# Optimization experiments

Hardware: AMD Instinct MI355X
Metric: run time of the kernel (lower is better)

## Reference

```python
import jax, jax.numpy as jnp
import numpy as np

B, S, D, H, DK = 2, 2048, 2048, 16, 128
ALIBI_SLOPE = 8.0
NEG = -1e9  # finite stand-in for -inf so gradients stay finite


def setup_inputs() -> dict:
    key = jax.random.key(0)
    ks = jax.random.split(key, 8)
    states = jax.random.normal(ks[0], (B, S, D), jnp.float32)
    # causal ALiBi-style additive bias: -(i-j) for j<=i else very negative
    pos = jnp.arange(S)
    dist = pos[None, :] - pos[:, None]  # j - i
    bias = jnp.where(dist <= 0, dist.astype(jnp.float32), NEG)
    bias_mask = jnp.broadcast_to(bias[None], (B, S, S))
    # per-head scale: exp2(-((h+1)*slope/H))
    head_scale = jnp.exp2(-((jnp.arange(H) + 1.0) * ALIBI_SLOPE / H)).astype(jnp.float32)
    init = lambda k, shp: jax.random.normal(k, shp, jnp.float32) * (shp[-1] ** -0.5)
    return {
        'states': states,
        'bias_mask': bias_mask,
        'head_scale': head_scale,
        'Wq': init(ks[1], (D, D)), 'bq': jnp.zeros((D,), jnp.float32),
        'Wk': init(ks[2], (D, D)), 'bk': jnp.zeros((D,), jnp.float32),
        'Wv': init(ks[3], (D, D)), 'bv': jnp.zeros((D,), jnp.float32),
        'Wg': init(ks[4], (H, D)), 'bg': jnp.zeros((H,), jnp.float32),
        'Wo': init(ks[5], (D, D)), 'bo': jnp.zeros((D,), jnp.float32),
    }


def reference(states, bias_mask, head_scale, Wq, bq, Wk, bk, Wv, bv, Wg, bg, Wo, bo):
    b, s, d = states.shape
    key_scale = DK ** -0.5
    proj = lambda x, W, bias: x @ W.T + bias
    # [b,s,d] -> [b,h,s,dk]
    q = proj(states, Wq, bq).reshape(b, s, H, DK).transpose(0, 2, 1, 3)
    k = proj(states, Wk, bk).reshape(b, s, H, DK).transpose(0, 2, 1, 3)
    v = proj(states, Wv, bv).reshape(b, s, H, DK).transpose(0, 2, 1, 3)
    # additive per-head ALiBi bias: [b,1,s,s] * [1,h,1,1]
    bias = bias_mask[:, None, :, :] * head_scale[None, :, None, None]
    scores = jnp.einsum('bhqd,bhkd->bhqk', q, k) * key_scale + bias
    attn = jax.nn.softmax(scores, axis=-1)
    o = jnp.einsum('bhqk,bhkd->bhqd', attn, v).transpose(0, 2, 1, 3)  # [b,s,h,dk]
    g = jax.nn.sigmoid(proj(states, Wg, bg))  # [b,s,h]
    o = o * g[..., None]
    return proj(o.reshape(b, s, d), Wo, bo)
```

## Files before the change

kernel.cpp:

```cpp
#include <hip/hip_runtime.h>

#define SEQ  2048
#define NROW 4096
#define KDIM 2048
#define NH   16
#define DKH  128
#define CSUB 20.0f
#define LOG2E 1.44269504088896f

typedef unsigned int u32;
typedef unsigned short u16;
typedef __attribute__((ext_vector_type(8))) __bf16 bf16x8;
typedef __attribute__((ext_vector_type(4))) float f32x4;
typedef __attribute__((ext_vector_type(4))) u16 u16x4;

struct alignas(16) U4 { u32 x, y, z, w; };

__device__ __forceinline__ u16 f2bf(float f) {
  u32 u = __builtin_bit_cast(u32, f);
  u32 r = (u + 0x7fffu + ((u >> 16) & 1u)) >> 16;
  return (u16)r;
}
__device__ __forceinline__ u16 f2bf_n(float f) {
  __bf16 h = (__bf16)f;
  return __builtin_bit_cast(u16, h);
}
__device__ __forceinline__ bf16x8 asb(U4 v) { return __builtin_bit_cast(bf16x8, v); }
__device__ __forceinline__ float exp2a(float x) {
  float r;
  asm("v_exp_f32 %0, %1" : "=v"(r) : "v"(x));
  return r;
}

__device__ __forceinline__ void gl2lds16(const u16* g, u16* l) {
  __builtin_amdgcn_global_load_lds(
      (const __attribute__((address_space(1))) void*)g,
      (__attribute__((address_space(3))) void*)l, 16, 0, 0);
}

__global__ __launch_bounds__(256)
void cvtk(const float* __restrict__ src, u16* __restrict__ dst, int n)
{
  const int i = (blockIdx.x * 256 + threadIdx.x) * 4;
  if (i < n) {
    f32x4 v = *(const f32x4*)(src + i);
    u16x4 o;
#pragma unroll
    for (int j = 0; j < 4; ++j) o[j] = f2bf_n(v[j]);
    *(u16x4*)(dst + i) = o;
  }
}

__global__ __launch_bounds__(256)
void cvt3k(const float* __restrict__ s0, const float* __restrict__ s1,
           const float* __restrict__ s2, u16* __restrict__ dst, int n)
{
  const float* s = blockIdx.y == 0 ? s0 : (blockIdx.y == 1 ? s1 : s2);
  u16* d = dst + (size_t)blockIdx.y * n;
  const int i = (blockIdx.x * 256 + threadIdx.x) * 4;
  if (i < n) {
    f32x4 v = *(const f32x4*)(s + i);
    u16x4 o;
#pragma unroll
    for (int j = 0; j < 4; ++j) o[j] = f2bf_n(v[j]);
    *(u16x4*)(d + i) = o;
  }
}

__global__ __launch_bounds__(512, 2)
void qkvg(const u16* __restrict__ A, const u16* __restrict__ B,
          const float* __restrict__ bq, const float* __restrict__ bk,
          const float* __restrict__ bv, u16* __restrict__ Qw,
          u16* __restrict__ Kw, u16* __restrict__ Vw)
{
  __shared__ alignas(16) u16 As[2][256 * 64];
  __shared__ alignas(16) u16 Bs[2][256 * 64];
  const int tid = threadIdx.x;
  const int lane = tid & 63, wave = tid >> 6;
  const int wm = wave >> 2, wn = wave & 3;
  const int l15 = lane & 15, quad = lane >> 4;
  const int l7 = l15 & 7;
  const int m0 = blockIdx.y * 256, n0 = blockIdx.x * 256;

  const int srow = wave * 8 + (lane >> 3);
  const int scol = ((lane & 7) ^ (lane >> 3)) * 8;

  f32x4 acc[8][4];
#pragma unroll
  for (int i = 0; i < 8; ++i)
#pragma unroll
    for (int j = 0; j < 4; ++j) acc[i][j] = {0.f, 0.f, 0.f, 0.f};

#define QSTAGE(kt, buf)                                                      \
  do {                                                                       \
    const int koff_ = (kt) * 64;                                             \
    _Pragma("unroll")                                                        \
    for (int j = 0; j < 4; ++j) {                                            \
      gl2lds16(A + (size_t)(m0 + j * 64 + srow) * KDIM + koff_ + scol,       \
               &As[buf][(j * 64 + wave * 8) * 64]);                          \
      gl2lds16(B + (size_t)(n0 + j * 64 + srow) * KDIM + koff_ + scol,       \
               &Bs[buf][(j * 64 + wave * 8) * 64]);                          \
    }                                                                        \
  } while (0)

  QSTAGE(0, 0);
  QSTAGE(1, 1);

  const int NT = KDIM / 64;
  for (int kt = 0; kt < NT; ++kt) {
    const int cb = kt & 1;
    if (kt + 1 < NT) asm volatile("s_waitcnt vmcnt(8)" ::: "memory");
    else             asm volatile("s_waitcnt vmcnt(0)" ::: "memory");
    asm volatile("s_barrier" ::: "memory");

    U4 bf[4][2];
#pragma unroll
    for (int nf = 0; nf < 4; ++nf)
#pragma unroll
      for (int kf = 0; kf < 2; ++kf)
        bf[nf][kf] = *(const U4*)(&Bs[cb][(wn * 64 + nf * 16 + l15) * 64 +
                                          (((kf * 4 + quad) ^ l7) * 8)]);
    __builtin_amdgcn_s_setprio(1);
#pragma unroll
    for (int p = 0; p < 4; ++p) {
      U4 af[2][2];
#pragma unroll
      for (int mi = 0; mi < 2; ++mi)
#pragma unroll
        for (int kf = 0; kf < 2; ++kf)
          af[mi][kf] = *(const U4*)(&As[cb][(wm * 128 + (p * 2 + mi) * 16 + l15) * 64 +
                                            (((kf * 4 + quad) ^ l7) * 8)]);
#pragma unroll
      for (int mi = 0; mi < 2; ++mi)
#pragma unroll
        for (int nf = 0; nf < 4; ++nf)
#pragma unroll
          for (int kf = 0; kf < 2; ++kf)
            acc[p * 2 + mi][nf] = __builtin_amdgcn_mfma_f32_16x16x32_bf16(
                asb(af[mi][kf]), asb(bf[nf][kf]), acc[p * 2 + mi][nf], 0, 0, 0);
    }
    __builtin_amdgcn_s_setprio(0);
    asm volatile("s_barrier" ::: "memory");
    if (kt + 2 < NT) QSTAGE(kt + 2, cb);
  }
#undef QSTAGE

  const int seg = n0 >> 11;
  const float* bp = seg == 0 ? bq : (seg == 1 ? bk : bv);
  u16* Cq = seg == 0 ? Qw : Kw;

#pragma unroll
  for (int mf = 0; mf < 8; ++mf) {
    const int rowb = m0 + wm * 128 + mf * 16 + quad * 4;
    const int b = rowb >> 11, sr = rowb & (SEQ - 1);
#pragma unroll
    for (int nf = 0; nf < 4; ++nf) {
      const int col6 = n0 + wn * 64 + nf * 16 + l15;
      const int col = col6 & 2047;
      const int h = col >> 7, dk = col & 127;
      const float bvl = bp[col];
      if (seg == 2) {
        u16x4 pk;
#pragma unroll
        for (int r = 0; r < 4; ++r) pk[r] = f2bf_n(acc[mf][nf][r] + bvl);
        *(u16x4*)(Vw + ((size_t)(b * NH + h) * DKH + dk) * SEQ + sr) = pk;
      } else {
#pragma unroll
        for (int r = 0; r < 4; ++r)
          Cq[((size_t)(b * NH + h) * SEQ + (sr + r)) * DKH + dk] =
              f2bf_n(acc[mf][nf][r] + bvl);
      }
    }
  }
}

__device__ __forceinline__ void stage_ab(const u16* __restrict__ A,
                                         const u16* __restrict__ B,
                                         int m0, int n0, int kk,
                                         u16* Asb, u16* Bsb,
                                         int wave, int gr, int gc)
{
#pragma unroll
  for (int it = 0; it < 2; ++it) {
    const int r0 = wave * 32 + it * 16;
    gl2lds16(A + (size_t)(m0 + r0 + gr) * KDIM + kk + gc, Asb + r0 * 32);
    gl2lds16(B + (size_t)(n0 + r0 + gr) * KDIM + kk + gc, Bsb + r0 * 32);
  }
}

__global__ __launch_bounds__(256, 2)
void gemm_bt(const u16* __restrict__ A, const u16* __restrict__ B,
             const float* __restrict__ bias, float* __restrict__ Cf)
{
  __shared__ alignas(16) u16 As[128 * 32];
  __shared__ alignas(16) u16 Bs[128 * 32];
  const int tid = threadIdx.x;
  const int lane = tid & 63, wave = tid >> 6;
  const int wm = wave >> 1, wn = wave & 1;
  const int l15 = lane & 15, quad = lane >> 4;
  const int m0 = blockIdx.y * 128, n0 = blockIdx.x * 128;

  f32x4 acc[4][4];
#pragma unroll
  for (int i = 0; i < 4; ++i)
#pragma unroll
    for (int j = 0; j < 4; ++j) acc[i][j] = {0.f, 0.f, 0.f, 0.f};

  const int gr = lane >> 2;
  const int gc = (lane & 3) * 8;

  for (int kk = 0; kk < KDIM; kk += 32) {
    stage_ab(A, B, m0, n0, kk, As, Bs, wave, gr, gc);
    __syncthreads();
    U4 af[4], bg[4];
#pragma unroll
    for (int t = 0; t < 4; ++t) {
      af[t] = *(const U4*)(As + (wm * 64 + t * 16 + l15) * 32 + quad * 8);
      bg[t] = *(const U4*)(Bs + (wn * 64 + t * 16 + l15) * 32 + quad * 8);
    }
#pragma unroll
    for (int mt = 0; mt < 4; ++mt)
#pragma unroll
      for (int nt = 0; nt < 4; ++nt)
        acc[mt][nt] = __builtin_amdgcn_mfma_f32_16x16x32_bf16(
            asb(af[mt]), asb(bg[nt]), acc[mt][nt], 0, 0, 0);
    __syncthreads();
  }

#pragma unroll
  for (int mt = 0; mt < 4; ++mt) {
    const int rowb = m0 + wm * 64 + mt * 16 + quad * 4;
#pragma unroll
    for (int nt = 0; nt < 4; ++nt) {
      const int col = n0 + wn * 64 + nt * 16 + l15;
      const float bv = bias[col];
#pragma unroll
      for (int r = 0; r < 4; ++r)
        Cf[(size_t)(rowb + r) * KDIM + col] = acc[mt][nt][r] + bv;
    }
  }
}

__global__ __launch_bounds__(256)
void gateg(const u16* __restrict__ X, const float* __restrict__ Wg,
           const float* __restrict__ bg, float* __restrict__ G)
{
  __shared__ float red[4][16][16];
  const int tid = threadIdx.x;
  const int lane = tid & 63, wave = tid >> 6;
  const int l15 = lane & 15, quad = lane >> 4;
  const int m0 = blockIdx.x * 16;

  const u16*  Xp = X + (size_t)(m0 + l15) * KDIM + wave * 512 + quad * 8;
  const float* Wp = Wg + (size_t)l15 * KDIM + wave * 512 + quad * 8;

  f32x4 acc = {0.f, 0.f, 0.f, 0.f};
#pragma unroll
  for (int kk = 0; kk < 512; kk += 32) {
    U4 a = *(const U4*)(Xp + kk);
    f32x4 w0 = *(const f32x4*)(Wp + kk);
    f32x4 w1 = *(const f32x4*)(Wp + kk + 4);
    U4 bw;
    bw.x = (u32)f2bf_n(w0[0]) | ((u32)f2bf_n(w0[1]) << 16);
    bw.y = (u32)f2bf_n(w0[2]) | ((u32)f2bf_n(w0[3]) << 16);
    bw.z = (u32)f2bf_n(w1[0]) | ((u32)f2bf_n(w1[1]) << 16);
    bw.w = (u32)f2bf_n(w1[2]) | ((u32)f2bf_n(w1[3]) << 16);
    acc = __builtin_amdgcn_mfma_f32_16x16x32_bf16(asb(a), asb(bw), acc, 0, 0, 0);
  }
#pragma unroll
  for (int r = 0; r < 4; ++r) red[wave][quad * 4 + r][l15] = acc[r];
  __syncthreads();
  const int row = tid >> 4, head = tid & 15;
  float s = bg[head];
#pragma unroll
  for (int w = 0; w < 4; ++w) s += red[w][row][head];
  G[(size_t)(m0 + row) * NH + head] = 1.f / (1.f + __expf(-s));
}

__device__ __forceinline__ void stage_kv(const u16* __restrict__ Kh,
                                         const u16* __restrict__ Vh,
                                         int kk, u16* Ksb, u16* Vsb,
                                         int wave, int lane)
{
  const int rK = lane >> 4, cK = lane & 15;
  const int rV = lane >> 3, cV = lane & 7;
#pragma unroll
  for (int j = 0; j < 4; ++j) {
    const int r0k = wave * 16 + j * 4;
    const int xk = ((j & 1) << 2) | rK;
    gl2lds16(Kh + (size_t)(kk + r0k + rK) * DKH + ((cK ^ xk) * 8),
             Ksb + r0k * 128);
    const int r0v = wave * 32 + j * 8;
    gl2lds16(Vh + (size_t)(r0v + rV) * SEQ + kk + ((cV ^ rV) * 8),
             Vsb + r0v * 64);
  }
}

__global__ __launch_bounds__(256, 2)
void attnk(const u16* __restrict__ Q, const u16* __restrict__ Km,
           const u16* __restrict__ Vt, const float* __restrict__ hsc,
           const float* __restrict__ G, u16* __restrict__ O)
{
  __shared__ alignas(16) u16 Ks[2][64 * 128];
  __shared__ alignas(16) u16 Vs[2][128 * 64];
  __shared__ alignas(16) u16 Ps[4][16 * 72];
  const int tid = threadIdx.x;
  const int lane = tid & 63, wave = tid >> 6;
  const int l15 = lane & 15, quad = lane >> 4;
  const int l7x = l15 & 7;
  const int qt = 31 - blockIdx.y, bh = blockIdx.x;
  const int b = bh >> 4, h = bh & 15;
  const size_t hoff = (size_t)bh * SEQ * DKH;
  const u16* Qh = Q + hoff;
  const u16* Kh = Km + hoff;
  const u16* Vh = Vt + hoff;
  const float hs2 = hsc[h] * LOG2E;
  const float ks2 = 0.08838834764831845f * LOG2E;
  const float csub2 = CSUB * LOG2E;
  const float dstep = 64.0f * hs2;

  const int q0 = qt * 64 + wave * 16;
  const int ntile = qt + 1;

  U4 aq[4];
#pragma unroll
  for (int c = 0; c < 4; ++c)
    aq[c] = *(const U4*)(Qh + (size_t)(q0 + l15) * DKH + c * 32 + quad * 8);

  float base[4][4];
#pragma unroll
  for (int r = 0; r < 4; ++r) {
    const int i = q0 + quad * 4 + r;
#pragma unroll
    for (int nt = 0; nt < 4; ++nt)
      base[r][nt] = (float)(nt * 16 + l15 - i) * hs2 - csub2;
  }

  f32x4 oacc[8];
#pragma unroll
  for (int c = 0; c < 8; ++c) oacc[c] = {0.f, 0.f, 0.f, 0.f};
  float l_lane[4] = {0.f, 0.f, 0.f, 0.f};

  stage_kv(Kh, Vh, 0, Ks[0], Vs[0], wave, lane);

  for (int t = 0; t < ntile; ++t) {
    const int kk = t * 64;
    const int cb = t & 1;
    __syncthreads();
    if (t + 1 < ntile)
      stage_kv(Kh, Vh, kk + 64, Ks[cb ^ 1], Vs[cb ^ 1], wave, lane);

    f32x4 sf[4];
#pragma unroll
    for (int nt = 0; nt < 4; ++nt) {
      f32x4 s = {0.f, 0.f, 0.f, 0.f};
#pragma unroll
      for (int c = 0; c < 4; ++c) {
        U4 bk = *(const U4*)(Ks[cb] + (nt * 16 + l15) * 128 +
                             (((c * 4 + quad) ^ l7x) * 8));
        s = __builtin_amdgcn_mfma_f32_16x16x32_bf16(asb(aq[c]), asb(bk), s, 0, 0, 0);
      }
      sf[nt] = s;
    }

    u16* Pw = &Ps[wave][0];
    const float tf = (float)t;
    if (t + 1 < ntile) {
#pragma unroll
      for (int r = 0; r < 4; ++r) {
#pragma unroll
        for (int nt = 0; nt < 4; ++nt) {
          const float p = exp2a(fmaf(sf[nt][r], ks2, fmaf(tf, dstep, base[r][nt])));
          l_lane[r] += p;
          Pw[(quad * 4 + r) * 72 + nt * 16 + l15] = f2bf_n(p);
        }
      }
    } else {
#pragma unroll
      for (int r = 0; r < 4; ++r) {
        const int i = q0 + quad * 4 + r;
#pragma unroll
        for (int nt = 0; nt < 4; ++nt) {
          const int j = kk + nt * 16 + l15;
          float p = 0.f;
          if (j <= i)
            p = exp2a(fmaf(sf[nt][r], ks2, fmaf(tf, dstep, base[r][nt])));
          l_lane[r] += p;
          Pw[(quad * 4 + r) * 72 + nt * 16 + l15] = f2bf_n(p);
        }
      }
    }
    asm volatile("s_waitcnt lgkmcnt(0)" ::: "memory");
    __builtin_amdgcn_sched_barrier(0);
    U4 pf0 = *(const U4*)(Pw + l15 * 72 + quad * 8);
    U4 pf1 = *(const U4*)(Pw + l15 * 72 + 32 + quad * 8);
#pragma unroll
    for (int c = 0; c < 8; ++c) {
      U4 bv0 = *(const U4*)(Vs[cb] + (c * 16 + l15) * 64 + ((quad ^ l7x) * 8));
      U4 bv1 = *(const U4*)(Vs[cb] + (c * 16 + l15) * 64 + (((quad + 4) ^ l7x) * 8));
      oacc[c] = __builtin_amdgcn_mfma_f32_16x16x32_bf16(asb(pf0), asb(bv0), oacc[c], 0, 0, 0);
      oacc[c] = __builtin_amdgcn_mfma_f32_16x16x32_bf16(asb(pf1), asb(bv1), oacc[c], 0, 0, 0);
    }
  }

  float sc[4];
#pragma unroll
  for (int r = 0; r < 4; ++r) {
#pragma unroll
    for (int d = 1; d < 16; d <<= 1)
      l_lane[r] += __shfl_xor(l_lane[r], d, 64);
    const int i = q0 + quad * 4 + r;
    sc[r] = G[(size_t)(b * SEQ + i) * NH + h] / l_lane[r];
  }

  __syncthreads();
  u16* OL = &Ks[0][0] + wave * 2112;
#pragma unroll
  for (int c = 0; c < 8; ++c)
#pragma unroll
    for (int r = 0; r < 4; ++r)
      OL[(quad * 4 + r) * 132 + c * 16 + l15] = f2bf_n(oacc[c][r] * sc[r]);
  __syncthreads();
#pragma unroll
  for (int o = 0; o < 4; ++o) {
    const int row = o * 4 + quad;
    U4 val = *(const U4*)(OL + row * 132 + l15 * 8);
    *(U4*)(O + ((size_t)(b * SEQ + q0 + row) * NH + h) * DKH + l15 * 8) = val;
  }
}

extern "C" void kernel_launch(void* const* d_in, const int* in_sizes, int n_in,
                              void* d_out, int out_size, void* d_ws, size_t ws_size,
                              hipStream_t stream)
{
  const float* states = (const float*)d_in[0];
  const float* hscale = (const float*)d_in[2];
  const float* Wq = (const float*)d_in[3];
  const float* bq = (const float*)d_in[4];
  const float* Wk = (const float*)d_in[5];
  const float* bk = (const float*)d_in[6];
  const float* Wv = (const float*)d_in[7];
  const float* bv = (const float*)d_in[8];
  const float* Wg = (const float*)d_in[9];
  const float* bg = (const float*)d_in[10];
  const float* Wo = (const float*)d_in[11];
  const float* bo = (const float*)d_in[12];
  float* out = (float*)d_out;

  char* ws = (char*)d_ws;
  const size_t MB = 1024 * 1024;
  u16* S16  = (u16*)(ws);
  u16* Qw   = (u16*)(ws + 16 * MB);
  u16* Kw   = (u16*)(ws + 32 * MB);
  u16* Vw   = (u16*)(ws + 48 * MB);
  u16* W16  = (u16*)(ws + 64 * MB);
  u16* Ow   = (u16*)(ws + 64 * MB);
  u16* Wo16 = (u16*)(ws + 80 * MB);
  float* Gw = out;

  const int NW = KDIM * KDIM;
  const int NS = NROW * KDIM;
  dim3 blk(256);

  cvtk<<<dim3(NS / 1024), blk, 0, stream>>>(states, S16, NS);
  gateg<<<dim3(NROW / 16), blk, 0, stream>>>(S16, Wg, bg, Gw);
  cvt3k<<<dim3(NW / 1024, 3), blk, 0, stream>>>(Wq, Wk, Wv, W16, NW);
  qkvg<<<dim3(24, 16), dim3(512), 0, stream>>>(S16, W16, bq, bk, bv, Qw, Kw, Vw);
  attnk<<<dim3(32, 32), blk, 0, stream>>>(Qw, Kw, Vw, hscale, Gw, Ow);
  cvtk<<<dim3(NW / 1024), blk, 0, stream>>>(Wo, Wo16, NW);
  gemm_bt<<<dim3(16, 32), blk, 0, stream>>>(Ow, Wo16, bo, out);
}
```

Baseline: 426.2 us.

## Unify QKV and output GEMMs into triple-buffered 256x128 kernel

Replaces the 256x256 double-buffered QKV GEMM and the simple 128x128 single-buffered output GEMM with one 8-wave 256x128 kernel. It uses a three-stage LDS ring and interleaves the next-tile global-to-LDS loads with the MFMA loop. A mode flag selects either the head-scattered bf16 QKV epilogue or the fp32 bias epilogue. The output projection gains prefetching and swizzled LDS, while the QKV GEMM gets smaller tiles, more blocks and a smaller register footprint, at the cost of more A-tile refetching.

```diff
diff --git a/kernel.cpp b/kernel.cpp
--- a/kernel.cpp
+++ b/kernel.cpp
@@ -68,137 +68,30 @@
 }
 
 __global__ __launch_bounds__(512, 2)
-void qkvg(const u16* __restrict__ A, const u16* __restrict__ B,
-          const float* __restrict__ bq, const float* __restrict__ bk,
-          const float* __restrict__ bv, u16* __restrict__ Qw,
-          u16* __restrict__ Kw, u16* __restrict__ Vw)
-{
-  __shared__ alignas(16) u16 As[2][256 * 64];
-  __shared__ alignas(16) u16 Bs[2][256 * 64];
-  const int tid = threadIdx.x;
-  const int lane = tid & 63, wave = tid >> 6;
-  const int wm = wave >> 2, wn = wave & 3;
-  const int l15 = lane & 15, quad = lane >> 4;
-  const int l7 = l15 & 7;
-  const int m0 = blockIdx.y * 256, n0 = blockIdx.x * 256;
-
-  const int srow = wave * 8 + (lane >> 3);
-  const int scol = ((lane & 7) ^ (lane >> 3)) * 8;
-
-  f32x4 acc[8][4];
-#pragma unroll
-  for (int i = 0; i < 8; ++i)
-#pragma unroll
-    for (int j = 0; j < 4; ++j) acc[i][j] = {0.f, 0.f, 0.f, 0.f};
-
-#define QSTAGE(kt, buf)                                                      \
-  do {                                                                       \
-    const int koff_ = (kt) * 64;                                             \
-    _Pragma("unroll")                                                        \
-    for (int j = 0; j < 4; ++j) {                                            \
-      gl2lds16(A + (size_t)(m0 + j * 64 + srow) * KDIM + koff_ + scol,       \
-               &As[buf][(j * 64 + wave * 8) * 64]);                          \
-      gl2lds16(B + (size_t)(n0 + j * 64 + srow) * KDIM + koff_ + scol,       \
-               &Bs[buf][(j * 64 + wave * 8) * 64]);                          \
-    }                                                                        \
-  } while (0)
-
-  QSTAGE(0, 0);
-  QSTAGE(1, 1);
-
-  const int NT = KDIM / 64;
-  for (int kt = 0; kt < NT; ++kt) {
-    const int cb = kt & 1;
-    if (kt + 1 < NT) asm volatile("s_waitcnt vmcnt(8)" ::: "memory");
-    else             asm volatile("s_waitcnt vmcnt(0)" ::: "memory");
-    asm volatile("s_barrier" ::: "memory");
-
-    U4 bf[4][2];
-#pragma unroll
-    for (int nf = 0; nf < 4; ++nf)
-#pragma unroll
-      for (int kf = 0; kf < 2; ++kf)
-        bf[nf][kf] = *(const U4*)(&Bs[cb][(wn * 64 + nf * 16 + l15) * 64 +
-                                          (((kf * 4 + quad) ^ l7) * 8)]);
-    __builtin_amdgcn_s_setprio(1);
-#pragma unroll
-    for (int p = 0; p < 4; ++p) {
-      U4 af[2][2];
-#pragma unroll
-      for (int mi = 0; mi < 2; ++mi)
-#pragma unroll
-        for (int kf = 0; kf < 2; ++kf)
-          af[mi][kf] = *(const U4*)(&As[cb][(wm * 128 + (p * 2 + mi) * 16 + l15) * 64 +
-                                            (((kf * 4 + quad) ^ l7) * 8)]);
-#pragma unroll
-      for (int mi = 0; mi < 2; ++mi)
-#pragma unroll
-        for (int nf = 0; nf < 4; ++nf)
-#pragma unroll
-          for (int kf = 0; kf < 2; ++kf)
-            acc[p * 2 + mi][nf] = __builtin_amdgcn_mfma_f32_16x16x32_bf16(
-                asb(af[mi][kf]), asb(bf[nf][kf]), acc[p * 2 + mi][nf], 0, 0, 0);
-    }
-    __builtin_amdgcn_s_setprio(0);
-    asm volatile("s_barrier" ::: "memory");
-    if (kt + 2 < NT) QSTAGE(kt + 2, cb);
-  }
-#undef QSTAGE
-
-  const int seg = n0 >> 11;
-  const float* bp = seg == 0 ? bq : (seg == 1 ? bk : bv);
-  u16* Cq = seg == 0 ? Qw : Kw;
-
-#pragma unroll
-  for (int mf = 0; mf < 8; ++mf) {
-    const int rowb = m0 + wm * 128 + mf * 16 + quad * 4;
-    const int b = rowb >> 11, sr = rowb & (SEQ - 1);
-#pragma unroll
-    for (int nf = 0; nf < 4; ++nf) {
-      const int col6 = n0 + wn * 64 + nf * 16 + l15;
-      const int col = col6 & 2047;
-      const int h = col >> 7, dk = col & 127;
-      const float bvl = bp[col];
-      if (seg == 2) {
-        u16x4 pk;
-#pragma unroll
-        for (int r = 0; r < 4; ++r) pk[r] = f2bf_n(acc[mf][nf][r] + bvl);
-        *(u16x4*)(Vw + ((size_t)(b * NH + h) * DKH + dk) * SEQ + sr) = pk;
-      } else {
-#pragma unroll
-        for (int r = 0; r < 4; ++r)
-          Cq[((size_t)(b * NH + h) * SEQ + (sr + r)) * DKH + dk] =
-              f2bf_n(acc[mf][nf][r] + bvl);
-      }
-    }
-  }
-}
-
-__device__ __forceinline__ void stage_ab(const u16* __restrict__ A,
-                                         const u16* __restrict__ B,
-                                         int m0, int n0, int kk,
-                                         u16* Asb, u16* Bsb,
-                                         int wave, int gr, int gc)
-{
-#pragma unroll
-  for (int it = 0; it < 2; ++it) {
-    const int r0 = wave * 32 + it * 16;
-    gl2lds16(A + (size_t)(m0 + r0 + gr) * KDIM + kk + gc, Asb + r0 * 32);
-    gl2lds16(B + (size_t)(n0 + r0 + gr) * KDIM + kk + gc, Bsb + r0 * 32);
-  }
-}
-
-__global__ __launch_bounds__(256, 2)
-void gemm_bt(const u16* __restrict__ A, const u16* __restrict__ B,
-             const float* __restrict__ bias, float* __restrict__ Cf)
-{
-  __shared__ alignas(16) u16 As[128 * 32];
-  __shared__ alignas(16) u16 Bs[128 * 32];
+void gemm8p(const u16* __restrict__ A, const u16* __restrict__ B,
+            const float* __restrict__ bq, const float* __restrict__ bk,
+            const float* __restrict__ bv, u16* __restrict__ Qw,
+            u16* __restrict__ Kw, u16* __restrict__ Vw,
+            float* __restrict__ Cf, int mode)
+{
+  __shared__ alignas(16) u16 As[3][256 * 64];
+  __shared__ alignas(16) u16 Bs[3][128 * 64];
   const int tid = threadIdx.x;
   const int lane = tid & 63, wave = tid >> 6;
   const int wm = wave >> 1, wn = wave & 1;
   const int l15 = lane & 15, quad = lane >> 4;
-  const int m0 = blockIdx.y * 128, n0 = blockIdx.x * 128;
+  const int l7 = l15 & 7;
+  const int m0 = blockIdx.y * 256, n0 = blockIdx.x * 128;
+
+  const int sr8 = lane >> 3;
+  const int scol = ((lane & 7) ^ sr8) * 8;
+
+#define STG_A(kt, buf, j)                                                    \
+  gl2lds16(A + (size_t)(m0 + (j) * 64 + wave * 8 + sr8) * KDIM + (kt) * 64 + scol, \
+           &As[buf][((j) * 64 + wave * 8) * 64])
+#define STG_B(kt, buf, j)                                                    \
+  gl2lds16(B + (size_t)(n0 + (j) * 64 + wave * 8 + sr8) * KDIM + (kt) * 64 + scol, \
+           &Bs[buf][((j) * 64 + wave * 8) * 64])
 
   f32x4 acc[4][4];
 #pragma unroll
@@ -206,37 +99,93 @@
 #pragma unroll
     for (int j = 0; j < 4; ++j) acc[i][j] = {0.f, 0.f, 0.f, 0.f};
 
-  const int gr = lane >> 2;
-  const int gc = (lane & 3) * 8;
-
-  for (int kk = 0; kk < KDIM; kk += 32) {
-    stage_ab(A, B, m0, n0, kk, As, Bs, wave, gr, gc);
-    __syncthreads();
-    U4 af[4], bg[4];
-#pragma unroll
-    for (int t = 0; t < 4; ++t) {
-      af[t] = *(const U4*)(As + (wm * 64 + t * 16 + l15) * 32 + quad * 8);
-      bg[t] = *(const U4*)(Bs + (wn * 64 + t * 16 + l15) * 32 + quad * 8);
-    }
-#pragma unroll
-    for (int mt = 0; mt < 4; ++mt)
-#pragma unroll
-      for (int nt = 0; nt < 4; ++nt)
-        acc[mt][nt] = __builtin_amdgcn_mfma_f32_16x16x32_bf16(
-            asb(af[mt]), asb(bg[nt]), acc[mt][nt], 0, 0, 0);
-    __syncthreads();
-  }
-
-#pragma unroll
-  for (int mt = 0; mt < 4; ++mt) {
-    const int rowb = m0 + wm * 64 + mt * 16 + quad * 4;
-#pragma unroll
-    for (int nt = 0; nt < 4; ++nt) {
-      const int col = n0 + wn * 64 + nt * 16 + l15;
-      const float bv = bias[col];
-#pragma unroll
-      for (int r = 0; r < 4; ++r)
-        Cf[(size_t)(rowb + r) * KDIM + col] = acc[mt][nt][r] + bv;
+  STG_A(0, 0, 0); STG_A(0, 0, 1); STG_A(0, 0, 2); STG_A(0, 0, 3);
+  STG_B(0, 0, 0); STG_B(0, 0, 1);
+  STG_A(1, 1, 0); STG_A(1, 1, 1); STG_A(1, 1, 2); STG_A(1, 1, 3);
+  STG_B(1, 1, 0); STG_B(1, 1, 1);
+
+  const int NT = KDIM / 64;
+  for (int kt = 0; kt < NT; ++kt) {
+    const int cb = kt % 3;
+    const int sb = (kt + 2) % 3;
+    if (kt + 1 < NT) asm volatile("s_waitcnt vmcnt(6)" ::: "memory");
+    else             asm volatile("s_waitcnt vmcnt(0)" ::: "memory");
+    asm volatile("s_barrier" ::: "memory");
+    __builtin_amdgcn_sched_barrier(0);
+    const bool st = (kt + 2) < NT;
+
+    U4 bf[4][2];
+#pragma unroll
+    for (int nf = 0; nf < 4; ++nf)
+#pragma unroll
+      for (int kf = 0; kf < 2; ++kf)
+        bf[nf][kf] = *(const U4*)(&Bs[cb][(wn * 64 + nf * 16 + l15) * 64 +
+                                          (((kf * 4 + quad) ^ l7) * 8)]);
+
+#pragma unroll
+    for (int mf = 0; mf < 4; ++mf) {
+      if (st) {
+        if (mf == 0) { STG_A(kt + 2, sb, 0); STG_A(kt + 2, sb, 1); }
+        else if (mf == 1) { STG_A(kt + 2, sb, 2); STG_A(kt + 2, sb, 3); }
+        else if (mf == 2) { STG_B(kt + 2, sb, 0); STG_B(kt + 2, sb, 1); }
+      }
+      U4 af[2];
+#pragma unroll
+      for (int kf = 0; kf < 2; ++kf)
+        af[kf] = *(const U4*)(&As[cb][(wm * 64 + mf * 16 + l15) * 64 +
+                                      (((kf * 4 + quad) ^ l7) * 8)]);
+      __builtin_amdgcn_s_setprio(1);
+#pragma unroll
+      for (int nf = 0; nf < 4; ++nf)
+#pragma unroll
+        for (int kf = 0; kf < 2; ++kf)
+          acc[mf][nf] = __builtin_amdgcn_mfma_f32_16x16x32_bf16(
+              asb(af[kf]), asb(bf[nf][kf]), acc[mf][nf], 0, 0, 0);
+      __builtin_amdgcn_s_setprio(0);
+    }
+  }
+#undef STG_A
+#undef STG_B
+
+  if (mode == 0) {
+#pragma unroll
+    for (int mf = 0; mf < 4; ++mf) {
+      const int rowb = m0 + wm * 64 + mf * 16 + quad * 4;
+#pragma unroll
+      for (int nf = 0; nf < 4; ++nf) {
+        const int col = n0 + wn * 64 + nf * 16 + l15;
+        const float bvl = bq[col];
+#pragma unroll
+        for (int r = 0; r < 4; ++r)
+          Cf[(size_t)(rowb + r) * KDIM + col] = acc[mf][nf][r] + bvl;
+      }
+    }
+  } else {
+    const int seg = n0 >> 11;
+    const float* bp = seg == 0 ? bq : (seg == 1 ? bk : bv);
+    u16* Cq = seg == 0 ? Qw : Kw;
+#pragma unroll
+    for (int mf = 0; mf < 4; ++mf) {
+      const int rowb = m0 + wm * 64 + mf * 16 + quad * 4;
+      const int b = rowb >> 11, sr = rowb & (SEQ - 1);
+#pragma unroll
+      for (int nf = 0; nf < 4; ++nf) {
+        const int col6 = n0 + wn * 64 + nf * 16 + l15;
+        const int col = col6 & 2047;
+        const int h = col >> 7, dk = col & 127;
+        const float bvl = bp[col];
+        if (seg == 2) {
+          u16x4 pk;
+#pragma unroll
+          for (int r = 0; r < 4; ++r) pk[r] = f2bf_n(acc[mf][nf][r] + bvl);
+          *(u16x4*)(Vw + ((size_t)(b * NH + h) * DKH + dk) * SEQ + sr) = pk;
+        } else {
+#pragma unroll
+          for (int r = 0; r < 4; ++r)
+            Cq[((size_t)(b * NH + h) * SEQ + (sr + r)) * DKH + dk] =
+                f2bf_n(acc[mf][nf][r] + bvl);
+        }
+      }
     }
   }
 }
@@ -465,8 +414,10 @@
   cvtk<<<dim3(NS / 1024), blk, 0, stream>>>(states, S16, NS);
   gateg<<<dim3(NROW / 16), blk, 0, stream>>>(S16, Wg, bg, Gw);
   cvt3k<<<dim3(NW / 1024, 3), blk, 0, stream>>>(Wq, Wk, Wv, W16, NW);
-  qkvg<<<dim3(24, 16), dim3(512), 0, stream>>>(S16, W16, bq, bk, bv, Qw, Kw, Vw);
+  gemm8p<<<dim3(48, 16), dim3(512), 0, stream>>>(S16, W16, bq, bk, bv,
+                                                 Qw, Kw, Vw, nullptr, 1);
+  cvtk<<<dim3(NW / 1024), blk, 0, stream>>>(Wo, Wo16, NW);
   attnk<<<dim3(32, 32), blk, 0, stream>>>(Qw, Kw, Vw, hscale, Gw, Ow);
-  cvtk<<<dim3(NW / 1024), blk, 0, stream>>>(Wo, Wo16, NW);
-  gemm_bt<<<dim3(16, 32), blk, 0, stream>>>(Ow, Wo16, bo, out);
-}
+  gemm8p<<<dim3(16, 16), dim3(512), 0, stream>>>(Ow, Wo16, bo, nullptr, nullptr,
+                                                 nullptr, nullptr, nullptr, out, 0);
+}
```

Measured after the change: 461.1 us. +8.2%, slower.
